# Performance work log

Measured on AMD Instinct MI355X. Metric: run time of the kernel, lower is better.

## Reference

```python
import jax, jax.numpy as jnp
import numpy as np


def relu_bt(x):
    # -threshold(-leaky_relu(x), -t, -t) == min(leaky_relu(x), t), t = ||x||_inf (detached)
    t = jax.lax.stop_gradient(jnp.max(jnp.abs(x)))
    return jnp.minimum(jax.nn.leaky_relu(x, negative_slope=0.01), t)


def setup_inputs() -> dict:
    key = jax.random.key(0)
    k1, k2, k3, k4 = jax.random.split(key, 4)
    N, E, F_in, F_out = 100000, 1600000, 128, 64
    x = jax.random.normal(k1, (N, F_in), dtype=jnp.float32)
    edge_index = jax.random.randint(k2, (2, E), 0, N, dtype=jnp.int64)
    # xavier_normal with gain=1.414
    W = jax.random.normal(k3, (F_in, F_out), dtype=jnp.float32) * (1.414 * np.sqrt(2.0 / (F_in + F_out)))
    a = jax.random.normal(k4, (1, 4 * F_out), dtype=jnp.float32) * (1.414 * np.sqrt(2.0 / (1 + 4 * F_out)))
    return {"x": x, "edge_index": edge_index, "W": W, "a": a}


def reference(x, edge_index, W, a):
    N = x.shape[0]
    F_out = W.shape[1]
    h = x @ W  # [N, F_out]
    src = edge_index[0]
    dst = edge_index[1]
    hs = h[src]  # [E, F_out]
    hd = h[dst]  # [E, F_out]
    agg = relu_bt(hs + hd)
    diff = relu_bt(hs - hd)
    # a @ cat([hs, hd, agg, diff], dim=1).T == sum of four per-edge dot products
    a0, a1, a2, a3 = jnp.split(a.reshape(4 * F_out), 4)
    score = hs @ a0 + hd @ a1 + agg @ a2 + diff @ a3  # [E]
    edge_e = jnp.exp(-relu_bt(score))  # [E]
    # spmm(A, ones): rowsum over outgoing edges (grouped by src)
    e_rowsum = jax.ops.segment_sum(edge_e, src, num_segments=N)  # [N]
    # spmm(A, h): weighted aggregation of neighbor (dst) features into src rows
    h_prime = jax.ops.segment_sum(edge_e[:, None] * hd, src, num_segments=N)  # [N, F_out]
    return h_prime / (e_rowsum[:, None] + 1e-16)
```

## Files before the change

### kernel.cpp

```cpp
#include <hip/hip_runtime.h>
#include <hip/hip_fp16.h>

#define F_IN 128
#define F_OUT 64
#define BIN_TILE 2048
#define BSHIFT 5
#define BNODES 32
#define BCAP 1024u

#define LK_A 0.505f
#define LK_B 0.495f

__device__ __forceinline__ float leaky(float v) {
    return fmaf(LK_B, fabsf(v), LK_A * v);
}

template <int CTRL>
__device__ __forceinline__ float dppadd(float v) {
    return v + __builtin_bit_cast(float,
        __builtin_amdgcn_update_dpp(0, __builtin_bit_cast(int, v), CTRL, 0xf, 0xf, true));
}

__device__ __forceinline__ float sum8(float v) {
    v = dppadd<0xB1>(v);
    v = dppadd<0x4E>(v);
    v = dppadd<0x141>(v);
    return v;
}

__device__ __forceinline__ float xslot_sum2(float v) {
    v = dppadd<0x128>(v);
    v += __shfl_xor(v, 16);
    return v;
}

__device__ __forceinline__ float wave_sum(float v) {
    v += __builtin_bit_cast(float, __builtin_amdgcn_update_dpp(0, __builtin_bit_cast(int, v), 0x111, 0xf, 0xf, true));
    v += __builtin_bit_cast(float, __builtin_amdgcn_update_dpp(0, __builtin_bit_cast(int, v), 0x112, 0xf, 0xf, true));
    v += __builtin_bit_cast(float, __builtin_amdgcn_update_dpp(0, __builtin_bit_cast(int, v), 0x114, 0xf, 0xe, true));
    v += __builtin_bit_cast(float, __builtin_amdgcn_update_dpp(0, __builtin_bit_cast(int, v), 0x118, 0xf, 0xc, true));
    v += __builtin_bit_cast(float, __builtin_amdgcn_update_dpp(0, __builtin_bit_cast(int, v), 0x142, 0xa, 0xf, true));
    v += __builtin_bit_cast(float, __builtin_amdgcn_update_dpp(0, __builtin_bit_cast(int, v), 0x143, 0xc, 0xf, true));
    return __builtin_bit_cast(float, __builtin_amdgcn_readlane(__builtin_bit_cast(int, v), 63));
}

__device__ __forceinline__ void cvt8(const uint4 u, float* g) {
    float2 f;
    f = __half22float2(__builtin_bit_cast(__half2, u.x)); g[0] = f.x; g[1] = f.y;
    f = __half22float2(__builtin_bit_cast(__half2, u.y)); g[2] = f.x; g[3] = f.y;
    f = __half22float2(__builtin_bit_cast(__half2, u.z)); g[4] = f.x; g[5] = f.y;
    f = __half22float2(__builtin_bit_cast(__half2, u.w)); g[6] = f.x; g[7] = f.y;
}

__device__ __forceinline__ float4 cvt4h(const uint2 u) {
    const float2 f0 = __half22float2(__builtin_bit_cast(__half2, u.x));
    const float2 f1 = __half22float2(__builtin_bit_cast(__half2, u.y));
    return make_float4(f0.x, f0.y, f1.x, f1.y);
}

__global__ __launch_bounds__(256) void gemm_binA(const float* __restrict__ x,
                                                 const float* __restrict__ W,
                                                 float* __restrict__ h32,
                                                 uint2* __restrict__ h16,
                                                 const int* __restrict__ ei,
                                                 unsigned* __restrict__ gcur,
                                                 unsigned* __restrict__ binned,
                                                 int N, int E, int NB, int ngemm,
                                                 unsigned cap, int mode) {
    __shared__ unsigned smem_u[4096];

    if ((int)blockIdx.x < ngemm) {
        __half2* wl = (__half2*)smem_u;
        for (int i = threadIdx.x; i < F_IN * F_OUT / 2; i += 256) {
            const float2 f = ((const float2*)W)[i];
            wl[i] = __floats2half2_rn(f.x, f.y);
        }
        __syncthreads();

        const int cg = threadIdx.x & 15;
        const int rs = threadIdx.x >> 4;
        const int row0 = blockIdx.x * 128 + rs * 8;

        int r[8];
#pragma unroll
        for (int i = 0; i < 8; ++i) { const int rr = row0 + i; r[i] = rr < N ? rr : N - 1; }

        float4 acc[8];
#pragma unroll
        for (int i = 0; i < 8; ++i) acc[i] = make_float4(0.f, 0.f, 0.f, 0.f);

        float4 xc[8];
#pragma unroll
        for (int i = 0; i < 8; ++i) xc[i] = *(const float4*)(x + (size_t)r[i] * F_IN);

        const char* wbase = (const char*)smem_u;
        for (int k4 = 0; k4 < 32; ++k4) {
            float4 xn[8];
            if (k4 < 31) {
#pragma unroll
                for (int i = 0; i < 8; ++i)
                    xn[i] = *(const float4*)(x + (size_t)r[i] * F_IN + (k4 + 1) * 4);
            }
            float4 wv[4];
#pragma unroll
            for (int kk = 0; kk < 4; ++kk) {
                const uint2 u = *(const uint2*)(wbase + ((k4 * 4 + kk) * 64 + cg * 4) * 2);
                wv[kk] = cvt4h(u);
            }

#pragma unroll
            for (int i = 0; i < 8; ++i) {
                acc[i].x = fmaf(xc[i].x, wv[0].x, acc[i].x);
                acc[i].y = fmaf(xc[i].x, wv[0].y, acc[i].y);
                acc[i].z = fmaf(xc[i].x, wv[0].z, acc[i].z);
                acc[i].w = fmaf(xc[i].x, wv[0].w, acc[i].w);
                acc[i].x = fmaf(xc[i].y, wv[1].x, acc[i].x);
                acc[i].y = fmaf(xc[i].y, wv[1].y, acc[i].y);
                acc[i].z = fmaf(xc[i].y, wv[1].z, acc[i].z);
                acc[i].w = fmaf(xc[i].y, wv[1].w, acc[i].w);
                acc[i].x = fmaf(xc[i].z, wv[2].x, acc[i].x);
                acc[i].y = fmaf(xc[i].z, wv[2].y, acc[i].y);
                acc[i].z = fmaf(xc[i].z, wv[2].z, acc[i].z);
                acc[i].w = fmaf(xc[i].z, wv[2].w, acc[i].w);
                acc[i].x = fmaf(xc[i].w, wv[3].x, acc[i].x);
                acc[i].y = fmaf(xc[i].w, wv[3].y, acc[i].y);
                acc[i].z = fmaf(xc[i].w, wv[3].z, acc[i].z);
                acc[i].w = fmaf(xc[i].w, wv[3].w, acc[i].w);
            }
            if (k4 < 31) {
#pragma unroll
                for (int i = 0; i < 8; ++i) xc[i] = xn[i];
            }
        }

#pragma unroll
        for (int i = 0; i < 8; ++i) {
            const int rr = row0 + i;
            if (rr < N) {
                if (mode & 2) *(float4*)(h32 + (size_t)rr * F_OUT + cg * 4) = acc[i];
                if (mode & 1) {
                    uint2 u;
                    u.x = __builtin_bit_cast(unsigned, __floats2half2_rn(acc[i].x, acc[i].y));
                    u.y = __builtin_bit_cast(unsigned, __floats2half2_rn(acc[i].z, acc[i].w));
                    h16[(size_t)rr * 16 + cg] = u;
                }
            }
        }
    } else {
        unsigned* lcnt = smem_u;
        const int t = threadIdx.x;
        for (int i = t; i < NB; i += 256) lcnt[i] = 0;
        __syncthreads();
        const int base = ((int)blockIdx.x - ngemm) * BIN_TILE;
        unsigned pk[8], bk[8], rk[8];
#pragma unroll
        for (int i = 0; i < 8; ++i) {
            const int e = base + i * 256 + t;
            if (e < E) {
                const unsigned s = (unsigned)ei[e];
                const unsigned d = (unsigned)ei[E + e];
                bk[i] = s >> BSHIFT;
                pk[i] = ((s & (BNODES - 1u)) << 17) | d;
                rk[i] = atomicAdd(&lcnt[bk[i]], 1u);
            }
        }
        __syncthreads();
        for (int i = t; i < NB; i += 256) {
            const unsigned c = lcnt[i];
            lcnt[i] = c ? atomicAdd(&gcur[i], c) : 0u;
        }
        __syncthreads();
#pragma unroll
        for (int i = 0; i < 8; ++i) {
            const int e = base + i * 256 + t;
            if (e < E) {
                const unsigned po = lcnt[bk[i]] + rk[i];
                if (po < cap) binned[(size_t)bk[i] * cap + po] = pk[i];
            }
        }
    }
}

__global__ __launch_bounds__(256) void bucket_node(const unsigned* __restrict__ binned,
                                                   const unsigned* __restrict__ gcur,
                                                   const uint2* __restrict__ h16v,
                                                   const float* __restrict__ a,
                                                   float* __restrict__ out,
                                                   int N, unsigned cap) {
    __shared__ unsigned stg[BCAP];
    __shared__ uint4    hsl[BNODES * 8];
    __shared__ unsigned ndeg[BNODES];
    __shared__ unsigned nbase[BNODES];
    __shared__ unsigned ncur[BNODES];

    const int b = blockIdx.x;
    const int t = threadIdx.x;
    const int node0 = b << BSHIFT;
    const size_t src0 = (size_t)b * cap;
    unsigned sz = gcur[b]; if (sz > cap) sz = cap;

    if (t < BNODES) ndeg[t] = 0;
    {
        const uint4* hsrc = (const uint4*)h16v;
        const int limit = N * 8;
        const int gi = node0 * 8 + t;
        hsl[t] = (gi < limit) ? hsrc[gi] : make_uint4(0u, 0u, 0u, 0u);
    }
    __syncthreads();

    for (unsigned i = t; i < sz; i += 256)
        atomicAdd(&ndeg[binned[src0 + i] >> 17], 1u);
    __syncthreads();

    if (t < BNODES) {
        const unsigned d = ndeg[t];
        unsigned sc = d;
#pragma unroll
        for (int st = 1; st < BNODES; st <<= 1) {
            const unsigned o = __shfl_up(sc, st, 64);
            if (t >= st) sc += o;
        }
        nbase[t] = sc - d;
        ncur[t]  = sc - d;
    }
    __syncthreads();

    for (unsigned i = t; i < sz; i += 256) {
        const unsigned p = binned[src0 + i];
        const unsigned pos = atomicAdd(&ncur[p >> 17], 1u);
        stg[pos] = p & 0x1FFFFu;
    }
    __syncthreads();

    const int lane  = t & 63;
    const int half  = lane >> 5;
    const int slot4 = (lane >> 3) & 3;
    const int q     = lane & 7;
    const int slot8 = (t >> 6) * 2 + half;
    const char* h16 = (const char*)h16v;

    float b1[8], a2b[8], a3b[8], a0m[8];
#pragma unroll
    for (int f = 0; f < 8; ++f) {
        const float A0 = a[q * 8 + f];
        const float A1 = a[64 + q * 8 + f];
        const float A2 = a[128 + q * 8 + f];
        const float A3 = a[192 + q * 8 + f];
        b1[f]  = fmaf(LK_A, A2 - A3, A1);
        a2b[f] = LK_B * A2;
        a3b[f] = LK_B * A3;
        a0m[f] = fmaf(LK_A, A2 + A3, A0);
    }

#pragma unroll 1
    for (int nn = 0; nn < BNODES / 8; ++nn) {
        const int nloc = slot8 * (BNODES / 8) + nn;
        const int node = node0 + nloc;
        const int beg = (int)nbase[nloc];
        const int len = (int)ndeg[nloc];

        float hs[8]; cvt8(hsl[nloc * 8 + q], hs);
        float csp = 0.f;
#pragma unroll
        for (int f = 0; f < 8; ++f) csp = fmaf(hs[f], a0m[f], csp);
        const float cs = sum8(csp);

        float acc[8];
#pragma unroll
        for (int f = 0; f < 8; ++f) acc[f] = 0.f;
        float rsum = 0.f;

        const int lm1 = (len > 0) ? len - 1 : 0;
        int dA = 0;
        if (len > 0) { int e0 = slot4; if (e0 > lm1) e0 = lm1; dA = (int)stg[beg + e0]; }
        uint4 uA = *(const uint4*)(h16 + ((size_t)dA << 7) + q * 16);
        int dB = dA;
        if (len > 4) { int e1 = 4 + slot4; if (e1 > lm1) e1 = lm1; dB = (int)stg[beg + e1]; }
        uint4 uB = *(const uint4*)(h16 + ((size_t)dB << 7) + q * 16);
        int dC = dB;
        if (len > 8) { int e2 = 8 + slot4; if (e2 > lm1) e2 = lm1; dC = (int)stg[beg + e2]; }

        for (int cb = 0; cb < len; cb += 4) {
            uint4 uC = uB;
            int dD = dC;
            if (cb + 8 < len)
                uC = *(const uint4*)(h16 + ((size_t)dC << 7) + q * 16);
            if (cb + 12 < len) { int e3 = cb + 12 + slot4; if (e3 > lm1) e3 = lm1; dD = (int)stg[beg + e3]; }

            float g[8];
            cvt8(uA, g);
            float p0 = 0.f, p1 = 0.f;
#pragma unroll
            for (int f = 0; f < 8; f += 2) {
                const float sa0 = hs[f] + g[f],         sb0 = hs[f] - g[f];
                const float sa1 = hs[f + 1] + g[f + 1], sb1 = hs[f + 1] - g[f + 1];
                p0 = fmaf(g[f],     b1[f],     p0);
                p1 = fmaf(g[f + 1], b1[f + 1], p1);
                p0 = fmaf(fabsf(sa0), a2b[f],     p0);
                p1 = fmaf(fabsf(sa1), a2b[f + 1], p1);
                p0 = fmaf(fabsf(sb0), a3b[f],     p0);
                p1 = fmaf(fabsf(sb1), a3b[f + 1], p1);
            }
            const float R = sum8(p0 + p1);

            float e = __expf(-leaky(cs + R));
            e = (cb + slot4 < len) ? e : 0.f;
#pragma unroll
            for (int f = 0; f < 8; ++f) acc[f] = fmaf(e, g[f], acc[f]);
            rsum += e;

            uA = uB; uB = uC; dC = dD;
        }

#pragma unroll
        for (int f = 0; f < 8; ++f) acc[f] = xslot_sum2(acc[f]);
        rsum = xslot_sum2(rsum);

        if (slot4 == 0 && node < N) {
            const float inv = 1.f / (rsum + 1e-16f);
            float4 o0, o1;
            o0.x = acc[0] * inv; o0.y = acc[1] * inv; o0.z = acc[2] * inv; o0.w = acc[3] * inv;
            o1.x = acc[4] * inv; o1.y = acc[5] * inv; o1.z = acc[6] * inv; o1.w = acc[7] * inv;
            float* orow = out + (size_t)node * F_OUT + q * 8;
            *(float4*)orow = o0;
            *(float4*)(orow + 4) = o1;
        }
    }
}

__global__ __launch_bounds__(256) void hist_kernel(const int* __restrict__ ei,
                                                   unsigned* __restrict__ cnt, int E) {
    const int e = blockIdx.x * 256 + threadIdx.x;
    if (e < E) atomicAdd(&cnt[ei[e]], 1u);
}

__global__ __launch_bounds__(256) void scan1(const unsigned* __restrict__ cnt,
                                             unsigned* __restrict__ bsum, int n) {
    __shared__ unsigned lds[256];
    const int t = threadIdx.x;
    const int base = blockIdx.x * 2048 + t * 8;
    unsigned s = 0;
#pragma unroll
    for (int i = 0; i < 8; ++i) { const int idx = base + i; if (idx < n) s += cnt[idx]; }
    lds[t] = s; __syncthreads();
    for (int st = 128; st > 0; st >>= 1) {
        if (t < st) lds[t] += lds[t + st];
        __syncthreads();
    }
    if (t == 0) bsum[blockIdx.x] = lds[0];
}

__global__ __launch_bounds__(128) void scan2(unsigned* __restrict__ bsum,
                                             unsigned* __restrict__ off, int nb, int n) {
    __shared__ unsigned lds[128];
    const int t = threadIdx.x;
    if (t < nb) lds[t] = bsum[t];
    __syncthreads();
    if (t == 0) {
        unsigned run = 0;
        for (int i = 0; i < nb; ++i) { const unsigned v = lds[i]; lds[i] = run; run += v; }
        off[n] = run;
    }
    __syncthreads();
    if (t < nb) bsum[t] = lds[t];
}

__global__ __launch_bounds__(256) void scan3(const unsigned* __restrict__ cnt,
                                             const unsigned* __restrict__ bsum,
                                             unsigned* __restrict__ off,
                                             unsigned* __restrict__ cursor, int n) {
    __shared__ unsigned lds[256];
    const int t = threadIdx.x;
    const int base = blockIdx.x * 2048 + t * 8;
    unsigned v[8]; unsigned s = 0;
#pragma unroll
    for (int i = 0; i < 8; ++i) { const int idx = base + i; v[i] = (idx < n) ? cnt[idx] : 0u; s += v[i]; }
    lds[t] = s; __syncthreads();
    for (int st = 1; st < 256; st <<= 1) {
        const unsigned add = (t >= st) ? lds[t - st] : 0u;
        __syncthreads();
        lds[t] += add;
        __syncthreads();
    }
    unsigned excl = (t > 0 ? lds[t - 1] : 0u) + bsum[blockIdx.x];
#pragma unroll
    for (int i = 0; i < 8; ++i) {
        const int idx = base + i;
        if (idx < n) { off[idx] = excl; cursor[idx] = excl; excl += v[i]; }
    }
}

__global__ __launch_bounds__(256) void scatter_kernel(const int* __restrict__ ei,
                                                      unsigned* __restrict__ cursor,
                                                      int* __restrict__ sdst, int E) {
    const int e = blockIdx.x * 256 + threadIdx.x;
    if (e >= E) return;
    const int s = ei[e];
    const int d = ei[E + e];
    const unsigned pos = atomicAdd(&cursor[s], 1u);
    sdst[pos] = d;
}

__global__ __launch_bounds__(256) void node_kernel(const unsigned* __restrict__ off,
                                                   const unsigned* __restrict__ deg,
                                                   const int* __restrict__ sdst,
                                                   const uint2* __restrict__ h16v,
                                                   const float* __restrict__ a,
                                                   float* __restrict__ out, int N) {
    const int lane  = threadIdx.x & 63;
    const int half  = lane >> 5;
    const int slot4 = (lane >> 3) & 3;
    const int q     = lane & 7;
    const char* h16 = (const char*)h16v;

    float b1[8], a2b[8], a3b[8], a0m[8];
#pragma unroll
    for (int f = 0; f < 8; ++f) {
        const float A0 = a[q * 8 + f];
        const float A1 = a[64 + q * 8 + f];
        const float A2 = a[128 + q * 8 + f];
        const float A3 = a[192 + q * 8 + f];
        b1[f]  = fmaf(LK_A, A2 - A3, A1);
        a2b[f] = LK_B * A2;
        a3b[f] = LK_B * A3;
        a0m[f] = fmaf(LK_A, A2 + A3, A0);
    }

    const int wid = (int)((blockIdx.x * 256u + threadIdx.x) >> 6);
    const int nw  = (int)((gridDim.x * 256u) >> 6);

    for (int pr = wid; pr * 2 < N; pr += nw) {
        const int node = pr * 2 + half;
        const int nc = (node < N) ? node : N - 1;
        const unsigned beg = off[nc];
        const int len = (node < N) ? (int)deg[nc] : 0;

        float hs[8];
        cvt8(*(const uint4*)(h16 + ((size_t)nc << 7) + q * 16), hs);
        float csp = 0.f;
#pragma unroll
        for (int f = 0; f < 8; ++f) csp = fmaf(hs[f], a0m[f], csp);
        const float cs = sum8(csp);

        const int lenO = __shfl_xor(len, 32);
        const int ml = (len > lenO) ? len : lenO;

        float acc[8];
#pragma unroll
        for (int f = 0; f < 8; ++f) acc[f] = 0.f;
        float rsum = 0.f;

        const int lm1 = (len > 0) ? len - 1 : 0;
        int dA = 0;
        if (len > 0) { int e0 = slot4; if (e0 > lm1) e0 = lm1; dA = sdst[beg + e0]; }
        uint4 uA = *(const uint4*)(h16 + ((size_t)dA << 7) + q * 16);
        int dB = dA;
        if (len > 4) { int e1 = 4 + slot4; if (e1 > lm1) e1 = lm1; dB = sdst[beg + e1]; }
        uint4 uB = *(const uint4*)(h16 + ((size_t)dB << 7) + q * 16);
        int dC = dB;
        if (len > 8) { int e2 = 8 + slot4; if (e2 > lm1) e2 = lm1; dC = sdst[beg + e2]; }

        for (int cb = 0; cb < ml; cb += 4) {
            uint4 uC = uB;
            int dD = dC;
            if (cb + 8 < len)
                uC = *(const uint4*)(h16 + ((size_t)dC << 7) + q * 16);
            if (cb + 12 < len) { int e3 = cb + 12 + slot4; if (e3 > lm1) e3 = lm1; dD = sdst[beg + e3]; }

            float g[8];
            cvt8(uA, g);
            float p0 = 0.f, p1 = 0.f;
#pragma unroll
            for (int f = 0; f < 8; f += 2) {
                const float sa0 = hs[f] + g[f],         sb0 = hs[f] - g[f];
                const float sa1 = hs[f + 1] + g[f + 1], sb1 = hs[f + 1] - g[f + 1];
                p0 = fmaf(g[f],     b1[f],     p0);
                p1 = fmaf(g[f + 1], b1[f + 1], p1);
                p0 = fmaf(fabsf(sa0), a2b[f],     p0);
                p1 = fmaf(fabsf(sa1), a2b[f + 1], p1);
                p0 = fmaf(fabsf(sb0), a3b[f],     p0);
                p1 = fmaf(fabsf(sb1), a3b[f + 1], p1);
            }
            const float R = sum8(p0 + p1);
            float e = __expf(-leaky(cs + R));
            e = (cb + slot4 < len) ? e : 0.f;
#pragma unroll
            for (int f = 0; f < 8; ++f) acc[f] = fmaf(e, g[f], acc[f]);
            rsum += e;
            uA = uB; uB = uC; dC = dD;
        }

#pragma unroll
        for (int f = 0; f < 8; ++f) acc[f] = xslot_sum2(acc[f]);
        rsum = xslot_sum2(rsum);

        if (slot4 == 0 && node < N) {
            const float inv = 1.f / (rsum + 1e-16f);
            float4 o0, o1;
            o0.x = acc[0] * inv; o0.y = acc[1] * inv; o0.z = acc[2] * inv; o0.w = acc[3] * inv;
            o1.x = acc[4] * inv; o1.y = acc[5] * inv; o1.z = acc[6] * inv; o1.w = acc[7] * inv;
            float* orow = out + (size_t)node * F_OUT + q * 8;
            *(float4*)orow = o0;
            *(float4*)(orow + 4) = o1;
        }
    }
}

__device__ __forceinline__ float edge_part(float hs, float hd, float a1, float a2, float a3) {
    float p = hd * a1;
    p = fmaf(leaky(hs + hd), a2, p);
    p = fmaf(leaky(hs - hd), a3, p);
    return p;
}

__global__ __launch_bounds__(256) void edge_kernel(const int* __restrict__ ei,
                                                   const float* __restrict__ h,
                                                   const float* __restrict__ a,
                                                   float* __restrict__ hprime,
                                                   float* __restrict__ rowsum,
                                                   int E) {
    const int lane = threadIdx.x & 63;
    const int wave = (int)((blockIdx.x * blockDim.x + threadIdx.x) >> 6);
    const int nwaves = (int)((gridDim.x * blockDim.x) >> 6);
    const float a0 = a[lane], a1 = a[64 + lane], a2 = a[128 + lane], a3 = a[192 + lane];
    for (int e = wave; e < E; e += nwaves) {
        const int s = ei[e];
        const int d = ei[E + e];
        const float hs = h[(size_t)s * F_OUT + lane];
        const float hd = h[(size_t)d * F_OUT + lane];
        const float part = wave_sum(hs * a0 + edge_part(hs, hd, a1, a2, a3));
        const float ee = __expf(-leaky(part));
        atomicAdd(&hprime[(size_t)s * F_OUT + lane], ee * hd);
        if (lane == 0) atomicAdd(&rowsum[s], ee);
    }
}

__global__ __launch_bounds__(256) void finalize(float* __restrict__ out,
                                                const float* __restrict__ rowsum,
                                                int total) {
    const int i = blockIdx.x * blockDim.x + threadIdx.x;
    if (i < total) out[i] = out[i] / (rowsum[i >> 6] + 1e-16f);
}

static inline size_t align_up(size_t v, size_t a) { return (v + a - 1) & ~(a - 1); }

extern "C" void kernel_launch(void* const* d_in, const int* in_sizes, int n_in,
                              void* d_out, int out_size, void* d_ws, size_t ws_size,
                              hipStream_t stream) {
    const float* x  = (const float*)d_in[0];
    const int*   ei = (const int*)d_in[1];
    const float* W  = (const float*)d_in[2];
    const float* a  = (const float*)d_in[3];

    const int N = in_sizes[0] / F_IN;
    const int E = in_sizes[1] / 2;
    float* out = (float*)d_out;

    const int NB = (N + BNODES - 1) >> BSHIFT;
    const int ngemm = (N + 127) / 128;
    const int nbt = (E + BIN_TILE - 1) / BIN_TILE;
    const unsigned meanFill = (NB > 0) ? (unsigned)(E / NB) : 0u;

    char* ws = (char*)d_ws;
    const size_t szh16  = align_up((size_t)N * F_OUT * 2, 256);
    const size_t szoff  = align_up(((size_t)N + 1) * 4, 256);
    const size_t szedge = align_up((size_t)E * 4 + 64, 256);
    const size_t szbin  = align_up((size_t)NB * BCAP * 4 + 64, 256);

    const size_t binned_b = szh16;
    const size_t gcurA_b  = binned_b + szbin;
    const size_t needA    = gcurA_b + align_up((size_t)NB * 4, 256);
    const size_t offB_b   = szh16;
    const size_t degB_b   = offB_b + szoff;
    const size_t sdstB_b  = degB_b + szoff;
    const size_t cursor_b = sdstB_b + szedge;
    const size_t bsum_b   = cursor_b + align_up((size_t)N * 4, 256);
    const size_t needB    = bsum_b + 4096;

    uint2* h16 = (uint2*)ws;

    if (ws_size >= needA && N <= (1 << 17) && NB <= 4096 && meanFill <= (BCAP * 3u) / 4u) {
        unsigned* binned = (unsigned*)(ws + binned_b);
        unsigned* gcur   = (unsigned*)(ws + gcurA_b);

        hipMemsetAsync(gcur, 0, (size_t)NB * 4, stream);
        gemm_binA<<<ngemm + nbt, 256, 0, stream>>>(x, W, nullptr, h16, ei, gcur, binned,
                                                   N, E, NB, ngemm, BCAP, 1);
        bucket_node<<<NB, 256, 0, stream>>>(binned, gcur, h16, a, out, N, BCAP);
    } else if (ws_size >= needB && N <= (1 << 17)) {
        unsigned* off    = (unsigned*)(ws + offB_b);
        unsigned* deg    = (unsigned*)(ws + degB_b);
        int*      sdst   = (int*)(ws + sdstB_b);
        unsigned* cursor = (unsigned*)(ws + cursor_b);
        unsigned* bsum   = (unsigned*)(ws + bsum_b);
        const int nb2 = (N + 2047) / 2048;

        hipMemsetAsync(deg, 0, (size_t)N * 4, stream);
        gemm_binA<<<ngemm, 256, 0, stream>>>(x, W, nullptr, h16, ei, nullptr, nullptr,
                                             N, E, NB, ngemm, BCAP, 1);
        hist_kernel<<<(E + 255) / 256, 256, 0, stream>>>(ei, deg, E);
        scan1<<<nb2, 256, 0, stream>>>(deg, bsum, N);
        scan2<<<1, 128, 0, stream>>>(bsum, off, nb2, N);
        scan3<<<nb2, 256, 0, stream>>>(deg, bsum, off, cursor, N);
        scatter_kernel<<<(E + 255) / 256, 256, 0, stream>>>(ei, cursor, sdst, E);
        node_kernel<<<2048, 256, 0, stream>>>(off, deg, sdst, h16, a, out, N);
    } else {
        float* h32    = (float*)ws;
        float* rowsum = (float*)(ws + align_up((size_t)N * F_OUT * 4, 256));
        hipMemsetAsync(d_out, 0, (size_t)N * F_OUT * sizeof(float), stream);
        hipMemsetAsync(rowsum, 0, (size_t)N * sizeof(float), stream);
        gemm_binA<<<ngemm, 256, 0, stream>>>(x, W, h32, nullptr, ei, nullptr, nullptr,
                                             N, E, NB, ngemm, BCAP, 2);
        edge_kernel<<<2048, 256, 0, stream>>>(ei, h32, a, out, rowsum, E);
        finalize<<<((size_t)N * F_OUT + 255) / 256, 256, 0, stream>>>(out, rowsum, N * F_OUT);
    }
}
```

Before: 135.2 us.

## Use few persistent binning blocks, fp32 W in LDS, 512-thread bucket kernel

```diff
diff --git a/kernel.cpp b/kernel.cpp
--- a/kernel.cpp
+++ b/kernel.cpp
@@ -3,10 +3,10 @@
 
 #define F_IN 128
 #define F_OUT 64
-#define BIN_TILE 2048
 #define BSHIFT 5
 #define BNODES 32
 #define BCAP 1024u
+#define NBIN_BLOCKS 64
 
 #define LK_A 0.505f
 #define LK_B 0.495f
@@ -52,12 +52,6 @@
     f = __half22float2(__builtin_bit_cast(__half2, u.w)); g[6] = f.x; g[7] = f.y;
 }
 
-__device__ __forceinline__ float4 cvt4h(const uint2 u) {
-    const float2 f0 = __half22float2(__builtin_bit_cast(__half2, u.x));
-    const float2 f1 = __half22float2(__builtin_bit_cast(__half2, u.y));
-    return make_float4(f0.x, f0.y, f1.x, f1.y);
-}
-
 __global__ __launch_bounds__(256) void gemm_binA(const float* __restrict__ x,
                                                  const float* __restrict__ W,
                                                  float* __restrict__ h32,
@@ -65,15 +59,16 @@
                                                  const int* __restrict__ ei,
                                                  unsigned* __restrict__ gcur,
                                                  unsigned* __restrict__ binned,
-                                                 int N, int E, int NB, int ngemm,
+                                                 int N, int E, int NB, int ngemm, int nbin,
                                                  unsigned cap, int mode) {
-    __shared__ unsigned smem_u[4096];
+    __shared__ unsigned smem_u[8192];
 
     if ((int)blockIdx.x < ngemm) {
-        __half2* wl = (__half2*)smem_u;
-        for (int i = threadIdx.x; i < F_IN * F_OUT / 2; i += 256) {
-            const float2 f = ((const float2*)W)[i];
-            wl[i] = __floats2half2_rn(f.x, f.y);
+        float (*w_lds)[F_OUT] = (float (*)[F_OUT])smem_u;
+        {
+            const float4* Wv = (const float4*)W;
+            float4* wl = (float4*)w_lds;
+            for (int i = threadIdx.x; i < F_IN * F_OUT / 4; i += 256) wl[i] = Wv[i];
         }
         __syncthreads();
 
@@ -93,7 +88,6 @@
 #pragma unroll
         for (int i = 0; i < 8; ++i) xc[i] = *(const float4*)(x + (size_t)r[i] * F_IN);
 
-        const char* wbase = (const char*)smem_u;
         for (int k4 = 0; k4 < 32; ++k4) {
             float4 xn[8];
             if (k4 < 31) {
@@ -103,10 +97,8 @@
             }
             float4 wv[4];
 #pragma unroll
-            for (int kk = 0; kk < 4; ++kk) {
-                const uint2 u = *(const uint2*)(wbase + ((k4 * 4 + kk) * 64 + cg * 4) * 2);
-                wv[kk] = cvt4h(u);
-            }
+            for (int kk = 0; kk < 4; ++kk)
+                wv[kk] = *(const float4*)&w_lds[k4 * 4 + kk][cg * 4];
 
 #pragma unroll
             for (int i = 0; i < 8; ++i) {
@@ -147,41 +139,38 @@
             }
         }
     } else {
-        unsigned* lcnt = smem_u;
+        unsigned* lcnt  = smem_u;
+        unsigned* lbase = smem_u + NB;
         const int t = threadIdx.x;
+        const int bi = (int)blockIdx.x - ngemm;
+        const int per = (E + nbin - 1) / nbin;
+        const int e0 = bi * per;
+        const int e1 = min(E, e0 + per);
+
         for (int i = t; i < NB; i += 256) lcnt[i] = 0;
         __syncthreads();
-        const int base = ((int)blockIdx.x - ngemm) * BIN_TILE;
-        unsigned pk[8], bk[8], rk[8];
-#pragma unroll
-        for (int i = 0; i < 8; ++i) {
-            const int e = base + i * 256 + t;
-            if (e < E) {
-                const unsigned s = (unsigned)ei[e];
-                const unsigned d = (unsigned)ei[E + e];
-                bk[i] = s >> BSHIFT;
-                pk[i] = ((s & (BNODES - 1u)) << 17) | d;
-                rk[i] = atomicAdd(&lcnt[bk[i]], 1u);
-            }
-        }
+        for (int e = e0 + t; e < e1; e += 256)
+            atomicAdd(&lcnt[((unsigned)ei[e]) >> BSHIFT], 1u);
         __syncthreads();
         for (int i = t; i < NB; i += 256) {
             const unsigned c = lcnt[i];
-            lcnt[i] = c ? atomicAdd(&gcur[i], c) : 0u;
-        }
-        __syncthreads();
-#pragma unroll
-        for (int i = 0; i < 8; ++i) {
-            const int e = base + i * 256 + t;
-            if (e < E) {
-                const unsigned po = lcnt[bk[i]] + rk[i];
-                if (po < cap) binned[(size_t)bk[i] * cap + po] = pk[i];
-            }
-        }
-    }
-}
-
-__global__ __launch_bounds__(256) void bucket_node(const unsigned* __restrict__ binned,
+            lbase[i] = c ? atomicAdd(&gcur[i], c) : 0u;
+        }
+        __syncthreads();
+        for (int i = t; i < NB; i += 256) lcnt[i] = 0;
+        __syncthreads();
+        for (int e = e0 + t; e < e1; e += 256) {
+            const unsigned s = (unsigned)ei[e];
+            const unsigned d = (unsigned)ei[E + e];
+            const unsigned bk = s >> BSHIFT;
+            const unsigned po = lbase[bk] + atomicAdd(&lcnt[bk], 1u);
+            if (po < cap)
+                binned[(size_t)bk * cap + po] = ((s & (BNODES - 1u)) << 17) | d;
+        }
+    }
+}
+
+__global__ __launch_bounds__(512) void bucket_node(const unsigned* __restrict__ binned,
                                                    const unsigned* __restrict__ gcur,
                                                    const uint2* __restrict__ h16v,
                                                    const float* __restrict__ a,
@@ -200,7 +189,7 @@
     unsigned sz = gcur[b]; if (sz > cap) sz = cap;
 
     if (t < BNODES) ndeg[t] = 0;
-    {
+    if (t < BNODES * 8) {
         const uint4* hsrc = (const uint4*)h16v;
         const int limit = N * 8;
         const int gi = node0 * 8 + t;
@@ -208,7 +197,7 @@
     }
     __syncthreads();
 
-    for (unsigned i = t; i < sz; i += 256)
+    for (unsigned i = t; i < sz; i += 512)
         atomicAdd(&ndeg[binned[src0 + i] >> 17], 1u);
     __syncthreads();
 
@@ -225,7 +214,7 @@
     }
     __syncthreads();
 
-    for (unsigned i = t; i < sz; i += 256) {
+    for (unsigned i = t; i < sz; i += 512) {
         const unsigned p = binned[src0 + i];
         const unsigned pos = atomicAdd(&ncur[p >> 17], 1u);
         stg[pos] = p & 0x1FFFFu;
@@ -236,7 +225,7 @@
     const int half  = lane >> 5;
     const int slot4 = (lane >> 3) & 3;
     const int q     = lane & 7;
-    const int slot8 = (t >> 6) * 2 + half;
+    const int proc  = (t >> 6) * 2 + half;
     const char* h16 = (const char*)h16v;
 
     float b1[8], a2b[8], a3b[8], a0m[8];
@@ -253,8 +242,8 @@
     }
 
 #pragma unroll 1
-    for (int nn = 0; nn < BNODES / 8; ++nn) {
-        const int nloc = slot8 * (BNODES / 8) + nn;
+    for (int nn = 0; nn < BNODES / 16; ++nn) {
+        const int nloc = proc * (BNODES / 16) + nn;
         const int node = node0 + nloc;
         const int beg = (int)nbase[nloc];
         const int len = (int)ndeg[nloc];
@@ -558,7 +547,7 @@
 
     const int NB = (N + BNODES - 1) >> BSHIFT;
     const int ngemm = (N + 127) / 128;
-    const int nbt = (E + BIN_TILE - 1) / BIN_TILE;
+    const int nbin = NBIN_BLOCKS;
     const unsigned meanFill = (NB > 0) ? (unsigned)(E / NB) : 0u;
 
     char* ws = (char*)d_ws;
@@ -584,9 +573,9 @@
         unsigned* gcur   = (unsigned*)(ws + gcurA_b);
 
         hipMemsetAsync(gcur, 0, (size_t)NB * 4, stream);
-        gemm_binA<<<ngemm + nbt, 256, 0, stream>>>(x, W, nullptr, h16, ei, gcur, binned,
-                                                   N, E, NB, ngemm, BCAP, 1);
-        bucket_node<<<NB, 256, 0, stream>>>(binned, gcur, h16, a, out, N, BCAP);
+        gemm_binA<<<ngemm + nbin, 256, 0, stream>>>(x, W, nullptr, h16, ei, gcur, binned,
+                                                    N, E, NB, ngemm, nbin, BCAP, 1);
+        bucket_node<<<NB, 512, 0, stream>>>(binned, gcur, h16, a, out, N, BCAP);
     } else if (ws_size >= needB && N <= (1 << 17)) {
         unsigned* off    = (unsigned*)(ws + offB_b);
         unsigned* deg    = (unsigned*)(ws + degB_b);
@@ -597,7 +586,7 @@
 
         hipMemsetAsync(deg, 0, (size_t)N * 4, stream);
         gemm_binA<<<ngemm, 256, 0, stream>>>(x, W, nullptr, h16, ei, nullptr, nullptr,
-                                             N, E, NB, ngemm, BCAP, 1);
+                                             N, E, NB, ngemm, nbin, BCAP, 1);
         hist_kernel<<<(E + 255) / 256, 256, 0, stream>>>(ei, deg, E);
         scan1<<<nb2, 256, 0, stream>>>(deg, bsum, N);
         scan2<<<1, 128, 0, stream>>>(bsum, off, nb2, N);
@@ -610,7 +599,7 @@
         hipMemsetAsync(d_out, 0, (size_t)N * F_OUT * sizeof(float), stream);
         hipMemsetAsync(rowsum, 0, (size_t)N * sizeof(float), stream);
         gemm_binA<<<ngemm, 256, 0, stream>>>(x, W, h32, nullptr, ei, nullptr, nullptr,
-                                             N, E, NB, ngemm, BCAP, 2);
+                                             N, E, NB, ngemm, nbin, BCAP, 2);
         edge_kernel<<<2048, 256, 0, stream>>>(ei, h32, a, out, rowsum, E);
         finalize<<<((size_t)N * F_OUT + 255) / 256, 256, 0, stream>>>(out, rowsum, N * F_OUT);
     }
```

New measurement: 188.0 us. +39.1%, slower.
